# Optimization experiments

Hardware: AMD Instinct MI355X
Metric: run time of the kernel (lower is better)

The kernel has to match this reference:

```python
import jax, jax.numpy as jnp
import numpy as np

MAGBIAS = 0.01


def _reflect_idx(l, m):
    # symmetric (edge-repeating) extension indices, length l + 2m, as in dtcwt reflect()
    x = np.arange(-m, l + m, dtype=np.float64)
    minx, maxx = -0.5, l - 0.5
    rng = maxx - minx
    mod = np.fmod(x - minx, 2.0 * rng)
    mod = np.where(mod < 0, mod + 2.0 * rng, mod)
    out = np.where(mod >= rng, 2.0 * rng - mod, mod) + minx
    return jnp.asarray(np.rint(out).astype(np.int64))


def _dwconv(x, h, axis, stride=1):
    # depthwise 1D correlation of (N,C,H,W) along spatial `axis` with 1D taps h, VALID
    C = x.shape[1]
    L = h.shape[0]
    if axis == 2:
        k = jnp.broadcast_to(h.reshape(1, 1, L, 1), (C, 1, L, 1))
        s = (stride, 1)
    else:
        k = jnp.broadcast_to(h.reshape(1, 1, 1, L), (C, 1, 1, L))
        s = (1, stride)
    return jax.lax.conv_general_dilated(
        x, k, s, 'VALID', dimension_numbers=('NCHW', 'OIHW', 'NCHW'),
        feature_group_count=C)


def _filt(x, h, axis):
    # level-1 non-decimated biort filter with symmetric boundary extension
    m = h.shape[0] // 2
    idx = _reflect_idx(x.shape[axis], m)
    return _dwconv(jnp.take(x, idx, axis=axis), h, axis)


def _dfilt(x, ha, hb, axis, highpass):
    # level-2+ decimated dual-tree qshift filter: tree a / tree b on alternate
    # phases of the symmetrically extended signal, outputs interleaved (order
    # swapped for highpass), decimating `axis` by 2 overall.
    n = x.shape[axis]
    m = ha.shape[0]
    idx = _reflect_idx(n, m)
    ya = _dwconv(jnp.take(x, idx[2::2], axis=axis), ha, axis, stride=2)  # n//4
    yb = _dwconv(jnp.take(x, idx[3::2], axis=axis), hb, axis, stride=2)  # n//4
    first, second = (yb, ya) if highpass else (ya, yb)
    y = jnp.stack((first, second), axis=axis + 1)
    shp = list(ya.shape)
    shp[axis] = n // 2
    return y.reshape(shp)


def _q2c(y):
    # quads -> two complex subimages: (a+jb)/2 + (d-jc)/2 and (a+jb)/2 - (d-jc)/2
    a = y[:, :, 0::2, 0::2]
    b = y[:, :, 0::2, 1::2]
    c = y[:, :, 1::2, 0::2]
    d = y[:, :, 1::2, 1::2]
    return ((a + d) * 0.5, (b - c) * 0.5), ((a - d) * 0.5, (b + c) * 0.5)


def _orientations(lh, hl, hh):
    (r15, i15), (r165, i165) = _q2c(lh)
    (r45, i45), (r135, i135) = _q2c(hh)
    (r75, i75), (r105, i105) = _q2c(hl)
    reals = jnp.stack([r15, r45, r75, r105, r135, r165], axis=1)
    imags = jnp.stack([i15, i45, i75, i105, i135, i165], axis=1)
    return reals, imags  # (N,6,C,h/2,w/2)


def _fwd_j1(x, h0, h1):
    lo = _filt(x, h0, 3)
    hi = _filt(x, h1, 3)
    ll = _filt(lo, h0, 2)
    lh = _filt(lo, h1, 2)
    hl = _filt(hi, h0, 2)
    hh = _filt(hi, h1, 2)
    reals, imags = _orientations(lh, hl, hh)
    return ll, reals, imags


def _fwd_j2(x, h0a, h0b, h1a, h1b):
    lo = _dfilt(x, h0a, h0b, 3, False)
    hi = _dfilt(x, h1a, h1b, 3, True)
    ll = _dfilt(lo, h0a, h0b, 2, False)
    lh = _dfilt(lo, h1a, h1b, 2, True)
    hl = _dfilt(hi, h0a, h0b, 2, False)
    hh = _dfilt(hi, h1a, h1b, 2, True)
    reals, imags = _orientations(lh, hl, hh)
    return ll, reals, imags


def _mag(r, i):
    return jnp.sqrt(r * r + i * i + MAGBIAS ** 2) - MAGBIAS


def _avg_pool2(x):
    n, c, h, w = x.shape
    return x.reshape(n, c, h // 2, 2, w // 2, 2).mean(axis=(3, 5))


def _forward(x, h0o, h1o, h0a, h0b, h1a, h1b):
    n, ch, H, W = x.shape  # H, W multiples of 8
    # first order, scale 1 (biort)
    s0, r, i = _fwd_j1(x, h0o, h1o)          # s0 (n,ch,H,W); highs (n,6,ch,H/2,W/2)
    s1_j1 = _mag(r, i)
    # first order, scale 2 (qshift)
    s0, r, i = _fwd_j2(s0, h0a, h0b, h1a, h1b)  # s0 (n,ch,H/2,W/2); highs H/4
    s1_j2 = _mag(r, i)
    s0 = _avg_pool2(s0)                      # (n,ch,H/4,W/4)
    # second order: scale-1 transform of the scale-1 magnitudes
    p = s1_j1.reshape(n, 6 * ch, H // 2, W // 2)
    p, r, i = _fwd_j1(p, h0o, h1o)
    s2 = _mag(r, i).reshape(n, 36, ch, H // 4, W // 4)
    s1_j1 = _avg_pool2(p).reshape(n, 6, ch, H // 4, W // 4)
    Z = jnp.concatenate([s0[:, None], s1_j1, s1_j2, s2], axis=1)  # (n,49,ch,H/4,W/4)
    return Z.reshape(n, 49 * ch, H // 4, W // 4)


def setup_inputs() -> dict:
    key = jax.random.key(0)
    ks = jax.random.split(key, 7)
    f32 = jnp.float32
    return {
        'x': jax.random.normal(ks[0], (8, 3, 512, 512), dtype=f32),
        'h0o': jax.random.normal(ks[1], (5,), dtype=f32) * 0.4,
        'h1o': jax.random.normal(ks[2], (7,), dtype=f32) * 0.4,
        'h0a': jax.random.normal(ks[3], (10,), dtype=f32) * 0.4,
        'h0b': jax.random.normal(ks[4], (10,), dtype=f32) * 0.4,
        'h1a': jax.random.normal(ks[5], (10,), dtype=f32) * 0.4,
        'h1b': jax.random.normal(ks[6], (10,), dtype=f32) * 0.4,
    }


def reference(x, h0o, h1o, h0a, h0b, h1a, h1b):
    return _forward(x, h0o, h1o, h0a, h0b, h1a, h1b)
```

## Files before the change

### kernel.cpp

```cpp
#include <hip/hip_runtime.h>
#include <math.h>

#define MAGB 0.01f

__device__ __forceinline__ int refl(int i, int n) {
  if (i < 0) i = -1 - i;
  if (i >= n) i = 2 * n - 1 - i;
  return i;
}

__device__ __forceinline__ float magf(float re, float im) {
  return sqrtf(re * re + im * im + MAGB * MAGB) - MAGB;
}

__device__ __forceinline__ void rowfilt4(const float* __restrict__ xr, int cb, int Wd,
                                         const float* __restrict__ f0,
                                         const float* __restrict__ f1,
                                         float* o0, float* o1) {
  float v[12];
  if (cb >= 4 && cb + 8 <= Wd) {
    float4 a = *(const float4*)(xr + cb - 4);
    float4 b = *(const float4*)(xr + cb);
    float4 c = *(const float4*)(xr + cb + 4);
    v[0] = a.x; v[1] = a.y; v[2] = a.z; v[3] = a.w;
    v[4] = b.x; v[5] = b.y; v[6] = b.z; v[7] = b.w;
    v[8] = c.x; v[9] = c.y; v[10] = c.z; v[11] = c.w;
  } else {
    v[0] = 0.f; v[11] = 0.f;
#pragma unroll
    for (int t = 1; t <= 10; ++t) v[t] = xr[refl(cb - 4 + t, Wd)];
  }
#pragma unroll
  for (int k = 0; k < 4; ++k) {
    float a0 = 0.f, a1 = 0.f;
#pragma unroll
    for (int j = 0; j < 5; ++j) a0 += f0[j] * v[k + 2 + j];
#pragma unroll
    for (int j = 0; j < 7; ++j) a1 += f1[j] * v[k + 1 + j];
    o0[k] = a0; o1[k] = a1;
  }
}

#define A_RF 38
#define A_PAD 68

struct J1Acc {
  float ll[2][4], lh[2][4], hl[2][4], hh[2][4];
};

__device__ __forceinline__ void j1_colfilt_pair(
    const float (*lo_s)[A_PAD], const float (*hi_s)[A_PAD],
    int h2l, int w2p, const float* __restrict__ f0, const float* __restrict__ f1,
    J1Acc* A) {
#pragma unroll
  for (int dr = 0; dr < 2; ++dr)
#pragma unroll
    for (int c = 0; c < 4; ++c) {
      A->ll[dr][c] = 0.f; A->lh[dr][c] = 0.f; A->hl[dr][c] = 0.f; A->hh[dr][c] = 0.f;
    }
#pragma unroll
  for (int tt = 0; tt < 8; ++tt) {
    float4 lv4 = *(const float4*)&lo_s[(h2l << 1) + tt][w2p << 2];
    float4 hv4 = *(const float4*)&hi_s[(h2l << 1) + tt][w2p << 2];
    float lv[4] = {lv4.x, lv4.y, lv4.z, lv4.w};
    float hv[4] = {hv4.x, hv4.y, hv4.z, hv4.w};
#pragma unroll
    for (int dr = 0; dr < 2; ++dr) {
      int j0 = tt - dr - 1;
      int j1 = tt - dr;
#pragma unroll
      for (int c = 0; c < 4; ++c) {
        if (j0 >= 0 && j0 < 5) {
          A->ll[dr][c] += f0[j0] * lv[c];
          A->hl[dr][c] += f0[j0] * hv[c];
        }
        if (j1 >= 0 && j1 < 7) {
          A->lh[dr][c] += f1[j1] * lv[c];
          A->hh[dr][c] += f1[j1] * hv[c];
        }
      }
    }
  }
}

__device__ __forceinline__ void q2c_mag_k(const float v[2][4], int k,
                                          float* mlo, float* mhi) {
  float a = v[0][2 * k], b = v[0][2 * k + 1], c = v[1][2 * k], d = v[1][2 * k + 1];
  *mlo = magf((a + d) * 0.5f, (b - c) * 0.5f);
  *mhi = magf((a - d) * 0.5f, (b + c) * 0.5f);
}

__global__ __launch_bounds__(256) void k_fused_j1a(
    const float* __restrict__ x,
    const float* __restrict__ h0, const float* __restrict__ h1,
    float* __restrict__ s0, float* __restrict__ pb) {
  constexpr int H = 512, W = 512;
  __shared__ float lo_s[A_RF][A_PAD];
  __shared__ float hi_s[A_RF][A_PAD];
  int p = blockIdx.x >> 7;
  int tloc = blockIdx.x & 127;
  int th = tloc >> 3, tw = tloc & 7;
  int h2_0 = th << 4, w2_0 = tw << 5;
  int c0 = w2_0 << 1;
  const float* xp = x + (size_t)p * (H * W);
  float f0[5], f1[7];
#pragma unroll
  for (int j = 0; j < 5; ++j) f0[j] = h0[j];
#pragma unroll
  for (int j = 0; j < 7; ++j) f1[j] = h1[j];
  int tid = threadIdx.x;

  for (int e = tid; e < A_RF * 16; e += 256) {
    int r = e >> 4, g = e & 15;
    int row = refl((h2_0 << 1) - 3 + r, H);
    const float* xr = xp + (size_t)row * W;
    float o0[4], o1[4];
    rowfilt4(xr, c0 + (g << 2), W, f0, f1, o0, o1);
    *(float4*)&lo_s[r][g << 2] = make_float4(o0[0], o0[1], o0[2], o0[3]);
    *(float4*)&hi_s[r][g << 2] = make_float4(o1[0], o1[1], o1[2], o1[3]);
  }
  __syncthreads();

  int n = p / 3, ch = p - 3 * n;
  float* s0p = s0 + (size_t)p * (H * W);
  constexpr size_t sp2 = 256 * 256;
  float* pbb = pb + (size_t)n * 18 * sp2;
  int h2l = tid >> 4, w2p = tid & 15;
  int h2 = h2_0 + h2l;
  int w2 = w2_0 + (w2p << 1);
  J1Acc A;
  j1_colfilt_pair(lo_s, hi_s, h2l, w2p, f0, f1, &A);
#pragma unroll
  for (int dr = 0; dr < 2; ++dr) {
    *(float4*)&s0p[(size_t)((h2 << 1) + dr) * W + (w2 << 1)] =
        make_float4(A.ll[dr][0], A.ll[dr][1], A.ll[dr][2], A.ll[dr][3]);
  }
  float m2[6][2];
#pragma unroll
  for (int k = 0; k < 2; ++k) {
    q2c_mag_k(A.lh, k, &m2[0][k], &m2[5][k]);
    q2c_mag_k(A.hh, k, &m2[1][k], &m2[4][k]);
    q2c_mag_k(A.hl, k, &m2[2][k], &m2[3][k]);
  }
#pragma unroll
  for (int o6 = 0; o6 < 6; ++o6) {
    *(float2*)&pbb[(size_t)(o6 * 3 + ch) * sp2 + ((size_t)h2 << 8) + w2] =
        make_float2(m2[o6][0], m2[o6][1]);
  }
}

#define B_R 80
#define B_PAD 36

__global__ __launch_bounds__(256) void k_fused_j2(
    const float* __restrict__ s0,
    const float* __restrict__ h0a, const float* __restrict__ h0b,
    const float* __restrict__ h1a, const float* __restrict__ h1b,
    float* __restrict__ out) {
  constexpr int H = 512, W = 512;
  __shared__ float lo2_s[B_R][B_PAD];
  __shared__ float hi2_s[B_R][B_PAD];
  int p = blockIdx.x >> 6;
  int tloc = blockIdx.x & 63;
  int th = tloc >> 3, tw = tloc & 7;
  int h4_0 = th << 4, w4_0 = tw << 4;
  const float* sp = s0 + (size_t)p * (H * W);
  float fa0[10], fb0[10], fa1[10], fb1[10];
#pragma unroll
  for (int j = 0; j < 10; ++j) {
    fa0[j] = h0a[j]; fb0[j] = h0b[j]; fa1[j] = h1a[j]; fb1[j] = h1b[j];
  }
  int tid = threadIdx.x;

  for (int e = tid; e < B_R * 8; e += 256) {
    int hr = e >> 3, g = e & 7;
    int row = refl((h4_0 << 2) - 8 + hr, H);
    const float* xr = sp + (size_t)row * W;
    int i0 = w4_0 + (g << 1);
    int base = (i0 << 2) - 8;
    float v[24];
    if (base >= 0 && base + 24 <= W) {
      const float* xb = xr + base;
#pragma unroll
      for (int q = 0; q < 6; ++q) {
        float4 t = *(const float4*)(xb + (q << 2));
        v[4 * q] = t.x; v[4 * q + 1] = t.y; v[4 * q + 2] = t.z; v[4 * q + 3] = t.w;
      }
    } else {
#pragma unroll
      for (int t = 0; t < 24; ++t) v[t] = xr[refl(base + t, W)];
    }
    float r0[4], r1[4];
#pragma unroll
    for (int k = 0; k < 2; ++k) {
      float ya0 = 0.f, yb0 = 0.f, ya1 = 0.f, yb1 = 0.f;
#pragma unroll
      for (int j = 0; j < 10; ++j) {
        float ve = v[4 * k + 2 * j], vo = v[4 * k + 2 * j + 1];
        ya0 += fa0[j] * ve; yb0 += fb0[j] * vo;
        ya1 += fa1[j] * ve; yb1 += fb1[j] * vo;
      }
      r0[2 * k] = ya0; r0[2 * k + 1] = yb0;
      r1[2 * k] = yb1; r1[2 * k + 1] = ya1;
    }
    *(float4*)&lo2_s[hr][g << 2] = make_float4(r0[0], r0[1], r0[2], r0[3]);
    *(float4*)&hi2_s[hr][g << 2] = make_float4(r1[0], r1[1], r1[2], r1[3]);
  }
  __syncthreads();

  {
    int h4l = tid >> 4, w4l = tid & 15;
    int h4 = h4_0 + h4l, w4 = w4_0 + w4l;
    int cl = w4l << 1;
    float a0l[2] = {0.f, 0.f}, b0l[2] = {0.f, 0.f}, a1l[2] = {0.f, 0.f}, b1l[2] = {0.f, 0.f};
    float a0h[2] = {0.f, 0.f}, b0h[2] = {0.f, 0.f}, a1h[2] = {0.f, 0.f}, b1h[2] = {0.f, 0.f};
#pragma unroll
    for (int j = 0; j < 10; ++j) {
      int hre = (h4l << 2) + 2 * j;
      float2 le = *(const float2*)&lo2_s[hre][cl];
      float2 lo_ = *(const float2*)&lo2_s[hre + 1][cl];
      float2 he = *(const float2*)&hi2_s[hre][cl];
      float2 ho = *(const float2*)&hi2_s[hre + 1][cl];
      a0l[0] += fa0[j] * le.x;  a0l[1] += fa0[j] * le.y;
      b0l[0] += fb0[j] * lo_.x; b0l[1] += fb0[j] * lo_.y;
      a1l[0] += fa1[j] * le.x;  a1l[1] += fa1[j] * le.y;
      b1l[0] += fb1[j] * lo_.x; b1l[1] += fb1[j] * lo_.y;
      a0h[0] += fa0[j] * he.x;  a0h[1] += fa0[j] * he.y;
      b0h[0] += fb0[j] * ho.x;  b0h[1] += fb0[j] * ho.y;
      a1h[0] += fa1[j] * he.x;  a1h[1] += fa1[j] * he.y;
      b1h[0] += fb1[j] * ho.x;  b1h[1] += fb1[j] * ho.y;
    }
    float llv[2][2], lhv[2][2], hlv[2][2], hhv[2][2];
#pragma unroll
    for (int dc = 0; dc < 2; ++dc) {
      llv[0][dc] = a0l[dc]; llv[1][dc] = b0l[dc];
      lhv[0][dc] = b1l[dc]; lhv[1][dc] = a1l[dc];
      hlv[0][dc] = a0h[dc]; hlv[1][dc] = b0h[dc];
      hhv[0][dc] = b1h[dc]; hhv[1][dc] = a1h[dc];
    }
    int n = p / 3, ch = p - 3 * n;
    constexpr size_t spo = 128 * 128;
    float* ob = out + (size_t)n * 147 * spo + ((size_t)h4 << 7) + w4;
    ob[(size_t)ch * spo] = 0.25f * (llv[0][0] + llv[0][1] + llv[1][0] + llv[1][1]);
    float m[6];
    { float a = lhv[0][0], b = lhv[0][1], c = lhv[1][0], d = lhv[1][1];
      m[0] = magf((a + d) * 0.5f, (b - c) * 0.5f);
      m[5] = magf((a - d) * 0.5f, (b + c) * 0.5f); }
    { float a = hhv[0][0], b = hhv[0][1], c = hhv[1][0], d = hhv[1][1];
      m[1] = magf((a + d) * 0.5f, (b - c) * 0.5f);
      m[4] = magf((a - d) * 0.5f, (b + c) * 0.5f); }
    { float a = hlv[0][0], b = hlv[0][1], c = hlv[1][0], d = hlv[1][1];
      m[2] = magf((a + d) * 0.5f, (b - c) * 0.5f);
      m[3] = magf((a - d) * 0.5f, (b + c) * 0.5f); }
#pragma unroll
    for (int o = 0; o < 6; ++o) {
      ob[(size_t)((7 + o) * 3 + ch) * spo] = m[o];
    }
  }
}

__global__ __launch_bounds__(256) void k_fused_j1c(
    const float* __restrict__ pb,
    const float* __restrict__ h0, const float* __restrict__ h1,
    float* __restrict__ out) {
  constexpr int H = 256, W = 256;
  __shared__ float lo_s[A_RF][A_PAD];
  __shared__ float hi_s[A_RF][A_PAD];
  int p = blockIdx.x >> 5;
  int tloc = blockIdx.x & 31;
  int th = tloc >> 2, tw = tloc & 3;
  int h2_0 = th << 4, w2_0 = tw << 5;
  int c0 = w2_0 << 1;
  const float* xp = pb + (size_t)p * (H * W);
  float f0[5], f1[7];
#pragma unroll
  for (int j = 0; j < 5; ++j) f0[j] = h0[j];
#pragma unroll
  for (int j = 0; j < 7; ++j) f1[j] = h1[j];
  int tid = threadIdx.x;

  for (int e = tid; e < A_RF * 16; e += 256) {
    int r = e >> 4, g = e & 15;
    int row = refl((h2_0 << 1) - 3 + r, H);
    const float* xr = xp + (size_t)row * W;
    float o0[4], o1[4];
    rowfilt4(xr, c0 + (g << 2), W, f0, f1, o0, o1);
    *(float4*)&lo_s[r][g << 2] = make_float4(o0[0], o0[1], o0[2], o0[3]);
    *(float4*)&hi_s[r][g << 2] = make_float4(o1[0], o1[1], o1[2], o1[3]);
  }
  __syncthreads();

  int c18 = p % 18, n = p / 18;
  int o1i = c18 / 3, ch = c18 - 3 * o1i;
  constexpr size_t spo = 128 * 128;
  float* ob = out + (size_t)n * 147 * spo;
  int h2l = tid >> 4, w2p = tid & 15;
  int h2 = h2_0 + h2l;
  int w2 = w2_0 + (w2p << 1);
  J1Acc A;
  j1_colfilt_pair(lo_s, hi_s, h2l, w2p, f0, f1, &A);
  size_t px = ((size_t)h2 << 7) + w2;
  float pl0 = 0.25f * (A.ll[0][0] + A.ll[0][1] + A.ll[1][0] + A.ll[1][1]);
  float pl1 = 0.25f * (A.ll[0][2] + A.ll[0][3] + A.ll[1][2] + A.ll[1][3]);
  *(float2*)&ob[(size_t)((1 + o1i) * 3 + ch) * spo + px] = make_float2(pl0, pl1);
  float m2[6][2];
#pragma unroll
  for (int k = 0; k < 2; ++k) {
    q2c_mag_k(A.lh, k, &m2[0][k], &m2[5][k]);
    q2c_mag_k(A.hh, k, &m2[1][k], &m2[4][k]);
    q2c_mag_k(A.hl, k, &m2[2][k], &m2[3][k]);
  }
#pragma unroll
  for (int o2 = 0; o2 < 6; ++o2) {
    *(float2*)&ob[(size_t)((13 + o2 * 6 + o1i) * 3 + ch) * spo + px] =
        make_float2(m2[o2][0], m2[o2][1]);
  }
}

extern "C" void kernel_launch(void* const* d_in, const int* in_sizes, int n_in,
                              void* d_out, int out_size, void* d_ws, size_t ws_size,
                              hipStream_t stream) {
  const float* x   = (const float*)d_in[0];
  const float* h0o = (const float*)d_in[1];
  const float* h1o = (const float*)d_in[2];
  const float* h0a = (const float*)d_in[3];
  const float* h0b = (const float*)d_in[4];
  const float* h1a = (const float*)d_in[5];
  const float* h1b = (const float*)d_in[6];
  float* out = (float*)d_out;
  char* ws = (char*)d_ws;
  (void)in_sizes; (void)n_in; (void)out_size; (void)ws_size;

  const size_t SZ_S0 = (size_t)24 * 512 * 512 * sizeof(float);
  float* s0 = (float*)ws;
  float* pb = (float*)(ws + SZ_S0);

  k_fused_j1a<<<3072, 256, 0, stream>>>(x, h0o, h1o, s0, pb);
  k_fused_j2<<<1536, 256, 0, stream>>>(s0, h0a, h0b, h1a, h1b, out);
  k_fused_j1c<<<4608, 256, 0, stream>>>(pb, h0o, h1o, out);
}
```

Baseline: 70.94 us.

## Store intermediate workspaces in fp16 and widen j1 tiles to 128 columns

The intermediate s0 lowpass image and the scale-1 magnitude buffer are written and read as half precision, with conversion to float on load. Global memory traffic between the three kernels drops by roughly half. The j1 kernels also process twice the width per block, with each thread computing two column groups, which cuts halo recomputation and block count. Reduced precision of the intermediates risks exceeding the accuracy tolerance, and the larger shared tiles may lower occupancy.

```diff
diff --git a/kernel.cpp b/kernel.cpp
--- a/kernel.cpp
+++ b/kernel.cpp
@@ -1,4 +1,5 @@
 #include <hip/hip_runtime.h>
+#include <hip/hip_fp16.h>
 #include <math.h>
 
 #define MAGB 0.01f
@@ -13,10 +14,25 @@
   return sqrtf(re * re + im * im + MAGB * MAGB) - MAGB;
 }
 
-__device__ __forceinline__ void rowfilt4(const float* __restrict__ xr, int cb, int Wd,
-                                         const float* __restrict__ f0,
-                                         const float* __restrict__ f1,
-                                         float* o0, float* o1) {
+__device__ __forceinline__ void filt4_win(const float* __restrict__ v,
+                                          const float* __restrict__ f0,
+                                          const float* __restrict__ f1,
+                                          float* o0, float* o1) {
+#pragma unroll
+  for (int k = 0; k < 4; ++k) {
+    float a0 = 0.f, a1 = 0.f;
+#pragma unroll
+    for (int j = 0; j < 5; ++j) a0 += f0[j] * v[k + 2 + j];
+#pragma unroll
+    for (int j = 0; j < 7; ++j) a1 += f1[j] * v[k + 1 + j];
+    o0[k] = a0; o1[k] = a1;
+  }
+}
+
+__device__ __forceinline__ void rowfilt4_f32(const float* __restrict__ xr, int cb, int Wd,
+                                             const float* __restrict__ f0,
+                                             const float* __restrict__ f1,
+                                             float* o0, float* o1) {
   float v[12];
   if (cb >= 4 && cb + 8 <= Wd) {
     float4 a = *(const float4*)(xr + cb - 4);
@@ -30,27 +46,35 @@
 #pragma unroll
     for (int t = 1; t <= 10; ++t) v[t] = xr[refl(cb - 4 + t, Wd)];
   }
+  filt4_win(v, f0, f1, o0, o1);
+}
+
+__device__ __forceinline__ void unpack8(float4 raw, float* dst) {
+  union { float4 f; __half2 h[4]; } u;
+  u.f = raw;
 #pragma unroll
   for (int k = 0; k < 4; ++k) {
-    float a0 = 0.f, a1 = 0.f;
-#pragma unroll
-    for (int j = 0; j < 5; ++j) a0 += f0[j] * v[k + 2 + j];
-#pragma unroll
-    for (int j = 0; j < 7; ++j) a1 += f1[j] * v[k + 1 + j];
-    o0[k] = a0; o1[k] = a1;
-  }
-}
-
-#define A_RF 38
-#define A_PAD 68
+    float2 t = __half22float2(u.h[k]);
+    dst[2 * k] = t.x; dst[2 * k + 1] = t.y;
+  }
+}
+
+__device__ __forceinline__ void st_half4(__half* dst, float a, float b, float c, float d) {
+  union { uint2 u; __half2 h[2]; } v;
+  v.h[0] = __floats2half2_rn(a, b);
+  v.h[1] = __floats2half2_rn(c, d);
+  *(uint2*)dst = v.u;
+}
+
+#define J1_STRIDE 132
 
 struct J1Acc {
   float ll[2][4], lh[2][4], hl[2][4], hh[2][4];
 };
 
-__device__ __forceinline__ void j1_colfilt_pair(
-    const float (*lo_s)[A_PAD], const float (*hi_s)[A_PAD],
-    int h2l, int w2p, const float* __restrict__ f0, const float* __restrict__ f1,
+__device__ __forceinline__ void j1_colfilt4(
+    const float* __restrict__ lo_s, const float* __restrict__ hi_s,
+    int row0, int col, const float* __restrict__ f0, const float* __restrict__ f1,
     J1Acc* A) {
 #pragma unroll
   for (int dr = 0; dr < 2; ++dr)
@@ -60,8 +84,8 @@
     }
 #pragma unroll
   for (int tt = 0; tt < 8; ++tt) {
-    float4 lv4 = *(const float4*)&lo_s[(h2l << 1) + tt][w2p << 2];
-    float4 hv4 = *(const float4*)&hi_s[(h2l << 1) + tt][w2p << 2];
+    float4 lv4 = *(const float4*)(lo_s + (row0 + tt) * J1_STRIDE + col);
+    float4 hv4 = *(const float4*)(hi_s + (row0 + tt) * J1_STRIDE + col);
     float lv[4] = {lv4.x, lv4.y, lv4.z, lv4.w};
     float hv[4] = {hv4.x, hv4.y, hv4.z, hv4.w};
 #pragma unroll
@@ -93,14 +117,14 @@
 __global__ __launch_bounds__(256) void k_fused_j1a(
     const float* __restrict__ x,
     const float* __restrict__ h0, const float* __restrict__ h1,
-    float* __restrict__ s0, float* __restrict__ pb) {
+    __half* __restrict__ s0, __half* __restrict__ pb) {
   constexpr int H = 512, W = 512;
-  __shared__ float lo_s[A_RF][A_PAD];
-  __shared__ float hi_s[A_RF][A_PAD];
-  int p = blockIdx.x >> 7;
-  int tloc = blockIdx.x & 127;
-  int th = tloc >> 3, tw = tloc & 7;
-  int h2_0 = th << 4, w2_0 = tw << 5;
+  __shared__ float lo_s[38 * J1_STRIDE];
+  __shared__ float hi_s[38 * J1_STRIDE];
+  int p = blockIdx.x >> 6;
+  int tloc = blockIdx.x & 63;
+  int th = tloc >> 2, tw = tloc & 3;
+  int h2_0 = th << 4, w2_0 = tw << 6;
   int c0 = w2_0 << 1;
   const float* xp = x + (size_t)p * (H * W);
   float f0[5], f1[7];
@@ -110,42 +134,46 @@
   for (int j = 0; j < 7; ++j) f1[j] = h1[j];
   int tid = threadIdx.x;
 
-  for (int e = tid; e < A_RF * 16; e += 256) {
-    int r = e >> 4, g = e & 15;
+  for (int e = tid; e < 38 * 32; e += 256) {
+    int r = e >> 5, g = e & 31;
     int row = refl((h2_0 << 1) - 3 + r, H);
     const float* xr = xp + (size_t)row * W;
     float o0[4], o1[4];
-    rowfilt4(xr, c0 + (g << 2), W, f0, f1, o0, o1);
-    *(float4*)&lo_s[r][g << 2] = make_float4(o0[0], o0[1], o0[2], o0[3]);
-    *(float4*)&hi_s[r][g << 2] = make_float4(o1[0], o1[1], o1[2], o1[3]);
+    rowfilt4_f32(xr, c0 + (g << 2), W, f0, f1, o0, o1);
+    *(float4*)&lo_s[r * J1_STRIDE + (g << 2)] = make_float4(o0[0], o0[1], o0[2], o0[3]);
+    *(float4*)&hi_s[r * J1_STRIDE + (g << 2)] = make_float4(o1[0], o1[1], o1[2], o1[3]);
   }
   __syncthreads();
 
   int n = p / 3, ch = p - 3 * n;
-  float* s0p = s0 + (size_t)p * (H * W);
-  constexpr size_t sp2 = 256 * 256;
-  float* pbb = pb + (size_t)n * 18 * sp2;
-  int h2l = tid >> 4, w2p = tid & 15;
-  int h2 = h2_0 + h2l;
-  int w2 = w2_0 + (w2p << 1);
-  J1Acc A;
-  j1_colfilt_pair(lo_s, hi_s, h2l, w2p, f0, f1, &A);
-#pragma unroll
-  for (int dr = 0; dr < 2; ++dr) {
-    *(float4*)&s0p[(size_t)((h2 << 1) + dr) * W + (w2 << 1)] =
-        make_float4(A.ll[dr][0], A.ll[dr][1], A.ll[dr][2], A.ll[dr][3]);
-  }
-  float m2[6][2];
-#pragma unroll
-  for (int k = 0; k < 2; ++k) {
-    q2c_mag_k(A.lh, k, &m2[0][k], &m2[5][k]);
-    q2c_mag_k(A.hh, k, &m2[1][k], &m2[4][k]);
-    q2c_mag_k(A.hl, k, &m2[2][k], &m2[3][k]);
-  }
-#pragma unroll
-  for (int o6 = 0; o6 < 6; ++o6) {
-    *(float2*)&pbb[(size_t)(o6 * 3 + ch) * sp2 + ((size_t)h2 << 8) + w2] =
-        make_float2(m2[o6][0], m2[o6][1]);
+  __half* s0p = s0 + (size_t)p * (H * W);
+  constexpr int sp2 = 256 * 256;
+  __half* pbb = pb + (size_t)n * 18 * sp2;
+  int hq = tid >> 4, wq = tid & 15;
+  int h2 = h2_0 + hq;
+#pragma unroll
+  for (int s = 0; s < 2; ++s) {
+    int colb = (wq << 2) + (s << 6);
+    int w2 = w2_0 + (wq << 1) + (s << 5);
+    J1Acc A;
+    j1_colfilt4(lo_s, hi_s, hq << 1, colb, f0, f1, &A);
+#pragma unroll
+    for (int dr = 0; dr < 2; ++dr) {
+      __half* d = s0p + (size_t)((h2 << 1) + dr) * W + c0 + colb;
+      st_half4(d, A.ll[dr][0], A.ll[dr][1], A.ll[dr][2], A.ll[dr][3]);
+    }
+    float m2[6][2];
+#pragma unroll
+    for (int k = 0; k < 2; ++k) {
+      q2c_mag_k(A.lh, k, &m2[0][k], &m2[5][k]);
+      q2c_mag_k(A.hh, k, &m2[1][k], &m2[4][k]);
+      q2c_mag_k(A.hl, k, &m2[2][k], &m2[3][k]);
+    }
+#pragma unroll
+    for (int o6 = 0; o6 < 6; ++o6) {
+      *(__half2*)&pbb[(size_t)(o6 * 3 + ch) * sp2 + (h2 << 8) + w2] =
+          __floats2half2_rn(m2[o6][0], m2[o6][1]);
+    }
   }
 }
 
@@ -153,7 +181,7 @@
 #define B_PAD 36
 
 __global__ __launch_bounds__(256) void k_fused_j2(
-    const float* __restrict__ s0,
+    const __half* __restrict__ s0,
     const float* __restrict__ h0a, const float* __restrict__ h0b,
     const float* __restrict__ h1a, const float* __restrict__ h1b,
     float* __restrict__ out) {
@@ -164,7 +192,7 @@
   int tloc = blockIdx.x & 63;
   int th = tloc >> 3, tw = tloc & 7;
   int h4_0 = th << 4, w4_0 = tw << 4;
-  const float* sp = s0 + (size_t)p * (H * W);
+  const __half* sp = s0 + (size_t)p * (H * W);
   float fa0[10], fb0[10], fa1[10], fb1[10];
 #pragma unroll
   for (int j = 0; j < 10; ++j) {
@@ -175,20 +203,18 @@
   for (int e = tid; e < B_R * 8; e += 256) {
     int hr = e >> 3, g = e & 7;
     int row = refl((h4_0 << 2) - 8 + hr, H);
-    const float* xr = sp + (size_t)row * W;
+    const __half* xr = sp + (size_t)row * W;
     int i0 = w4_0 + (g << 1);
     int base = (i0 << 2) - 8;
     float v[24];
     if (base >= 0 && base + 24 <= W) {
-      const float* xb = xr + base;
-#pragma unroll
-      for (int q = 0; q < 6; ++q) {
-        float4 t = *(const float4*)(xb + (q << 2));
-        v[4 * q] = t.x; v[4 * q + 1] = t.y; v[4 * q + 2] = t.z; v[4 * q + 3] = t.w;
-      }
+      const float4* xb = (const float4*)(xr + base);
+      unpack8(xb[0], v);
+      unpack8(xb[1], v + 8);
+      unpack8(xb[2], v + 16);
     } else {
 #pragma unroll
-      for (int t = 0; t < 24; ++t) v[t] = xr[refl(base + t, W)];
+      for (int t = 0; t < 24; ++t) v[t] = __half2float(xr[refl(base + t, W)]);
     }
     float r0[4], r1[4];
 #pragma unroll
@@ -239,7 +265,7 @@
       hhv[0][dc] = b1h[dc]; hhv[1][dc] = a1h[dc];
     }
     int n = p / 3, ch = p - 3 * n;
-    constexpr size_t spo = 128 * 128;
+    constexpr int spo = 128 * 128;
     float* ob = out + (size_t)n * 147 * spo + ((size_t)h4 << 7) + w4;
     ob[(size_t)ch * spo] = 0.25f * (llv[0][0] + llv[0][1] + llv[1][0] + llv[1][1]);
     float m[6];
@@ -260,18 +286,18 @@
 }
 
 __global__ __launch_bounds__(256) void k_fused_j1c(
-    const float* __restrict__ pb,
+    const __half* __restrict__ pb,
     const float* __restrict__ h0, const float* __restrict__ h1,
     float* __restrict__ out) {
   constexpr int H = 256, W = 256;
-  __shared__ float lo_s[A_RF][A_PAD];
-  __shared__ float hi_s[A_RF][A_PAD];
-  int p = blockIdx.x >> 5;
-  int tloc = blockIdx.x & 31;
-  int th = tloc >> 2, tw = tloc & 3;
-  int h2_0 = th << 4, w2_0 = tw << 5;
+  __shared__ float lo_s[38 * J1_STRIDE];
+  __shared__ float hi_s[38 * J1_STRIDE];
+  int p = blockIdx.x >> 4;
+  int tloc = blockIdx.x & 15;
+  int th = tloc >> 1, tw = tloc & 1;
+  int h2_0 = th << 4, w2_0 = tw << 6;
   int c0 = w2_0 << 1;
-  const float* xp = pb + (size_t)p * (H * W);
+  const __half* xp = pb + (size_t)p * (H * W);
   float f0[5], f1[7];
 #pragma unroll
   for (int j = 0; j < 5; ++j) f0[j] = h0[j];
@@ -279,41 +305,59 @@
   for (int j = 0; j < 7; ++j) f1[j] = h1[j];
   int tid = threadIdx.x;
 
-  for (int e = tid; e < A_RF * 16; e += 256) {
-    int r = e >> 4, g = e & 15;
+  for (int e = tid; e < 38 * 32; e += 256) {
+    int r = e >> 5, g = e & 31;
     int row = refl((h2_0 << 1) - 3 + r, H);
-    const float* xr = xp + (size_t)row * W;
+    const __half* xr = xp + (size_t)row * W;
+    int cb = c0 + (g << 2);
     float o0[4], o1[4];
-    rowfilt4(xr, c0 + (g << 2), W, f0, f1, o0, o1);
-    *(float4*)&lo_s[r][g << 2] = make_float4(o0[0], o0[1], o0[2], o0[3]);
-    *(float4*)&hi_s[r][g << 2] = make_float4(o1[0], o1[1], o1[2], o1[3]);
+    if (cb >= 8 && cb + 8 <= W) {
+      int base8 = (cb - 4) & ~7;
+      float hv[16];
+      unpack8(*(const float4*)(xr + base8), hv);
+      unpack8(*(const float4*)(xr + base8 + 8), hv + 8);
+      if (g & 1) filt4_win(hv, f0, f1, o0, o1);
+      else       filt4_win(hv + 4, f0, f1, o0, o1);
+    } else {
+      float v[12];
+      v[0] = 0.f; v[11] = 0.f;
+#pragma unroll
+      for (int t = 1; t <= 10; ++t) v[t] = __half2float(xr[refl(cb - 4 + t, W)]);
+      filt4_win(v, f0, f1, o0, o1);
+    }
+    *(float4*)&lo_s[r * J1_STRIDE + (g << 2)] = make_float4(o0[0], o0[1], o0[2], o0[3]);
+    *(float4*)&hi_s[r * J1_STRIDE + (g << 2)] = make_float4(o1[0], o1[1], o1[2], o1[3]);
   }
   __syncthreads();
 
   int c18 = p % 18, n = p / 18;
   int o1i = c18 / 3, ch = c18 - 3 * o1i;
-  constexpr size_t spo = 128 * 128;
+  constexpr int spo = 128 * 128;
   float* ob = out + (size_t)n * 147 * spo;
-  int h2l = tid >> 4, w2p = tid & 15;
-  int h2 = h2_0 + h2l;
-  int w2 = w2_0 + (w2p << 1);
-  J1Acc A;
-  j1_colfilt_pair(lo_s, hi_s, h2l, w2p, f0, f1, &A);
-  size_t px = ((size_t)h2 << 7) + w2;
-  float pl0 = 0.25f * (A.ll[0][0] + A.ll[0][1] + A.ll[1][0] + A.ll[1][1]);
-  float pl1 = 0.25f * (A.ll[0][2] + A.ll[0][3] + A.ll[1][2] + A.ll[1][3]);
-  *(float2*)&ob[(size_t)((1 + o1i) * 3 + ch) * spo + px] = make_float2(pl0, pl1);
-  float m2[6][2];
-#pragma unroll
-  for (int k = 0; k < 2; ++k) {
-    q2c_mag_k(A.lh, k, &m2[0][k], &m2[5][k]);
-    q2c_mag_k(A.hh, k, &m2[1][k], &m2[4][k]);
-    q2c_mag_k(A.hl, k, &m2[2][k], &m2[3][k]);
-  }
-#pragma unroll
-  for (int o2 = 0; o2 < 6; ++o2) {
-    *(float2*)&ob[(size_t)((13 + o2 * 6 + o1i) * 3 + ch) * spo + px] =
-        make_float2(m2[o2][0], m2[o2][1]);
+  int hq = tid >> 4, wq = tid & 15;
+  int h2 = h2_0 + hq;
+#pragma unroll
+  for (int s = 0; s < 2; ++s) {
+    int colb = (wq << 2) + (s << 6);
+    int w2 = w2_0 + (wq << 1) + (s << 5);
+    J1Acc A;
+    j1_colfilt4(lo_s, hi_s, hq << 1, colb, f0, f1, &A);
+    size_t px = ((size_t)h2 << 7) + w2;
+    float pl0 = 0.25f * (A.ll[0][0] + A.ll[0][1] + A.ll[1][0] + A.ll[1][1]);
+    float pl1 = 0.25f * (A.ll[0][2] + A.ll[0][3] + A.ll[1][2] + A.ll[1][3]);
+    *(float2*)&ob[(size_t)((1 + o1i) * 3 + ch) * spo + px] = make_float2(pl0, pl1);
+    float m2[6][2];
+#pragma unroll
+    for (int k = 0; k < 2; ++k) {
+      q2c_mag_k(A.lh, k, &m2[0][k], &m2[5][k]);
+      q2c_mag_k(A.hh, k, &m2[1][k], &m2[4][k]);
+      q2c_mag_k(A.hl, k, &m2[2][k], &m2[3][k]);
+    }
+#pragma unroll
+    for (int o2 = 0; o2 < 6; ++o2) {
+      *(float2*)&ob[(size_t)((13 + o2 * 6 + o1i) * 3 + ch) * spo + px] =
+          make_float2(m2[o2][0], m2[o2][1]);
+    }
   }
 }
 
@@ -331,11 +375,11 @@
   char* ws = (char*)d_ws;
   (void)in_sizes; (void)n_in; (void)out_size; (void)ws_size;
 
-  const size_t SZ_S0 = (size_t)24 * 512 * 512 * sizeof(float);
-  float* s0 = (float*)ws;
-  float* pb = (float*)(ws + SZ_S0);
-
-  k_fused_j1a<<<3072, 256, 0, stream>>>(x, h0o, h1o, s0, pb);
+  const size_t SZ_S0 = (size_t)24 * 512 * 512 * sizeof(__half);
+  __half* s0 = (__half*)ws;
+  __half* pb = (__half*)(ws + SZ_S0);
+
+  k_fused_j1a<<<1536, 256, 0, stream>>>(x, h0o, h1o, s0, pb);
   k_fused_j2<<<1536, 256, 0, stream>>>(s0, h0a, h0b, h1a, h1b, out);
-  k_fused_j1c<<<4608, 256, 0, stream>>>(pb, h0o, h1o, out);
-}
+  k_fused_j1c<<<2304, 256, 0, stream>>>(pb, h0o, h1o, out);
+}
```

Measured after the change: 77.06 us. 8.6% more time.
